# Performance work log

Measured on AMD Instinct MI355X. Metric: run time of the kernel, lower is better.

The kernel has to match this reference:

```python
import jax, jax.numpy as jnp
import numpy as np


def _rotated_kernels(kernel, n_or):
    """Nearest-neighbour rotated copies of the kernel.

    kernel: [C, kOr, kH, kW] -> returns [n_or, C, kOr, kH, kW] where slice t is the
    kernel sampled at R_{2*pi*t/n_or}(y', x') about the kernel center; rotated
    coordinates that fall outside the kernel grid contribute zero.
    """
    C, kOr, kH, kW = kernel.shape
    cy = (kH - 1) / 2.0
    cx = (kW - 1) / 2.0
    ang = 2.0 * jnp.pi * jnp.arange(n_or, dtype=jnp.float32) / n_or
    ca = jnp.cos(ang)[:, None, None]  # [n_or,1,1]
    sa = jnp.sin(ang)[:, None, None]
    yy = jnp.arange(kH, dtype=jnp.float32)[:, None] - cy  # [kH,1]
    xx = jnp.arange(kW, dtype=jnp.float32)[None, :] - cx  # [1,kW]
    # rotate grid points by angle theta
    ys = sa * xx + ca * yy  # [n_or,kH,kW]
    xs = ca * xx - sa * yy
    iy = jnp.round(ys + cy).astype(jnp.int32)
    ix = jnp.round(xs + cx).astype(jnp.int32)
    mask = ((iy >= 0) & (iy < kH) & (ix >= 0) & (ix < kW)).astype(kernel.dtype)
    iyc = jnp.clip(iy, 0, kH - 1)
    ixc = jnp.clip(ix, 0, kW - 1)
    rot = kernel[:, :, iyc, ixc]            # [C,kOr,n_or,kH,kW] (gather)
    rot = rot * mask[None, None]            # zero out-of-grid samples
    return jnp.transpose(rot, (2, 0, 1, 3, 4))  # [n_or,C,kOr,kH,kW]


def setup_inputs() -> dict:
    key = jax.random.key(0)
    k1, k2 = jax.random.split(key)
    B, C, Or, H, W = 8, 32, 8, 128, 128
    kOr, kH, kW = 8, 5, 5
    x = jax.random.normal(k1, (B, C, Or, H, W), dtype=jnp.float32)
    # module parameter: uniform(-1, 1) per reset_parameters()
    kernel = jax.random.uniform(k2, (C, kOr, kH, kW), minval=-1.0, maxval=1.0,
                                dtype=jnp.float32)
    return {"x": x, "kernel": kernel}


def reference(x, kernel):
    """SE(2) linear (depthwise) group convolution.

    out[b,c,t,y,x] = sum_{t',y',x'} x[b,c,(t+t')%Or, y+y', x+x']
                     * kernel[c, t', NN(R_{2pi t/Or}(y', x'))]
    with centered, zero-padded spatial offsets ('SAME').
    """
    B, C, Or, H, W = x.shape
    _, kOr, kH, kW = kernel.shape
    rotk = _rotated_kernels(kernel, Or)  # [Or,C,kOr,kH,kW]
    dn = ('NCHW', 'OIHW', 'NCHW')
    out = jnp.zeros((B, C * Or, H, W), dtype=x.dtype)
    for tp in range(kOr):  # small fixed orientation-offset loop
        xs = jnp.roll(x, -tp, axis=2).reshape(B, C * Or, H, W)  # circular wrap in Or
        k = jnp.transpose(rotk[:, :, tp], (1, 0, 2, 3)).reshape(C * Or, 1, kH, kW)
        out = out + jax.lax.conv_general_dilated(
            xs, k, window_strides=(1, 1), padding='SAME',
            feature_group_count=C * Or, dimension_numbers=dn)
    return out.reshape(B, C, Or, H, W)
```

## Files before the change

### kernel.cpp

```cpp
#include <hip/hip_runtime.h>


typedef short bf16x8 __attribute__((ext_vector_type(8)));
typedef float f32x4 __attribute__((ext_vector_type(4)));

#define EPIL_TS 1092
#define EPIL_RP 68

__device__ inline unsigned short f2bf(float f) {
    unsigned int u = __float_as_uint(f);
    u += 0x7fffu + ((u >> 16) & 1u);
    return (unsigned short)(u >> 16);
}
__device__ inline unsigned pk2(float a, float b) {
    return (unsigned)f2bf(a) | ((unsigned)f2bf(b) << 16);
}

__device__ __constant__ float CA8[8] = {1.0f, 0.70710678f, 0.0f, -0.70710678f,
                                        -1.0f, -0.70710678f, 0.0f, 0.70710678f};
__device__ __constant__ float SA8[8] = {0.0f, 0.70710678f, 1.0f, 0.70710678f,
                                        0.0f, -0.70710678f, -1.0f, -0.70710678f};

__device__ inline float rot_w(const float* __restrict__ kern, int c, int t,
                              int o, int dy, int dx) {
    float ca = CA8[t], sa = SA8[t];
    float xx = (float)dx - 2.0f, yy = (float)dy - 2.0f;
    int iy = (int)rintf(sa * xx + ca * yy + 2.0f);
    int ix = (int)rintf(ca * xx - sa * yy + 2.0f);
    if (iy >= 0 && iy < 5 && ix >= 0 && ix < 5) {
        int tp = (o - t) & 7;
        return kern[(c * 8 + tp) * 25 + iy * 5 + ix];
    }
    return 0.0f;
}

__global__ __launch_bounds__(256)
void build_w2(const float* __restrict__ kern, unsigned short* __restrict__ wtab) {
    int e = blockIdx.x * 256 + threadIdx.x;
    if (e >= 131072) return;
    int o   = e & 7;
    int tr  = (e >> 3) & 31;
    int n16 = (e >> 8) & 15;
    int c   = e >> 12;
    int t   = n16 & 7, dlt = n16 >> 3;
    float w = 0.0f;
    if (tr < 30) {
        int dyr = tr / 5, dx = tr - 5 * dyr;
        int dy  = dyr - dlt;
        if (dy >= 0 && dy < 5) w = rot_w(kern, c, t, o, dy, dx);
    }
    wtab[e] = f2bf(w);
}

template <bool TAB>
__global__ __launch_bounds__(256)
void se2_mfma(const float* __restrict__ x, const float* __restrict__ kern,
              const unsigned short* __restrict__ wtab, float* __restrict__ out) {
    __shared__ __align__(16) float ldsbuf[8 * EPIL_TS];
    unsigned short* stage = reinterpret_cast<unsigned short*>(ldsbuf);
    float* epil = ldsbuf;

    const int bid = (blockIdx.x & 7) * 512 + (blockIdx.x >> 3);
    const int xh2 = bid & 1;
    const int ys  = (bid >> 1) & 7;
    const int bc  = bid >> 4;
    const int c   = bc & 31;
    const int X0  = xh2 * 64, Y0 = ys * 16;
    const int tid = threadIdx.x;

    const int lane = tid & 63;
    const int wv   = tid >> 6;
    const int g    = lane >> 4;
    const int m16  = lane & 15;

    const float* xbase = x + (size_t)bc * 131072;

    auto loadch = [&](int e, float (&v)[8]) {
        int r = e / 68, col = e - r * 68;
        int gy = Y0 - 2 + r, gx = X0 - 2 + col;
        if (gy >= 0 && gy < 128 && gx >= 0 && gx < 128) {
            const float* src = xbase + gy * 128 + gx;
#pragma unroll
            for (int o = 0; o < 8; ++o) v[o] = src[o * 16384];
        } else {
#pragma unroll
            for (int o = 0; o < 8; ++o) v[o] = 0.0f;
        }
    };
    auto packch = [&](int e, const float (&v)[8]) {
        *reinterpret_cast<uint4*>(&stage[e * 8]) =
            make_uint4(pk2(v[0], v[1]), pk2(v[2], v[3]),
                       pk2(v[4], v[5]), pk2(v[6], v[7]));
    };

    float v0[8], v1[8], v2[8], v3[8], v4[8], v5[8];
    loadch(tid, v0);
    loadch(tid + 256, v1);
    loadch(tid + 512, v2);
    loadch(tid + 768, v3);
    loadch(tid + 1024, v4);
    if (tid < 80) loadch(tid + 1280, v5);

    bf16x8 wfrag[8];
    int    tapoff[8];
#pragma unroll
    for (int cc = 0; cc < 8; ++cc) {
        int tr  = cc * 4 + g;
        int trc = tr < 30 ? tr : 29;
        int dyr = trc / 5, dx = trc - 5 * dyr;
        tapoff[cc] = (dyr * 68 + dx) * 8;
        if constexpr (TAB)
            wfrag[cc] = *reinterpret_cast<const bf16x8*>(
                &wtab[((c * 16 + m16) * 32 + tr) * 8]);
    }

    if constexpr (!TAB) {
        unsigned short* ldsw = stage + 12288;
        for (int e = tid; e < 4096; e += 256) {
            int o = e & 7, tr = (e >> 3) & 31, n16 = e >> 8;
            int t = n16 & 7, dlt = n16 >> 3;
            float w = 0.0f;
            if (tr < 30) {
                int dyr = tr / 5, dx = tr - 5 * dyr;
                int dy  = dyr - dlt;
                if (dy >= 0 && dy < 5) w = rot_w(kern, c, t, o, dy, dx);
            }
            ldsw[e] = f2bf(w);
        }
        __syncthreads();
#pragma unroll
        for (int cc = 0; cc < 8; ++cc)
            wfrag[cc] = *reinterpret_cast<const bf16x8*>(
                &ldsw[(m16 * 32 + cc * 4 + g) * 8]);
        __syncthreads();
    }

    packch(tid, v0);
    packch(tid + 256, v1);
    packch(tid + 512, v2);
    packch(tid + 768, v3);
    packch(tid + 1024, v4);
    if (tid < 80) packch(tid + 1280, v5);
    __syncthreads();

    f32x4 acc[8];
#pragma unroll
    for (int s = 0; s < 8; ++s) {
        acc[s] = (f32x4){0.f, 0.f, 0.f, 0.f};
        const int yl = wv * 4 + (s >> 2) * 2;
        const int baseS = (yl * 68 + (s & 3) * 16 + m16) * 8;
#pragma unroll
        for (int cc = 0; cc < 8; ++cc) {
            bf16x8 xf = *reinterpret_cast<const bf16x8*>(&stage[baseS + tapoff[cc]]);
            acc[s] = __builtin_amdgcn_mfma_f32_16x16x32_bf16(xf, wfrag[cc], acc[s], 0, 0, 0);
        }
    }
    __syncthreads();

    const int t_o = m16 & 7, dlt = m16 >> 3;
#pragma unroll
    for (int s = 0; s < 8; ++s) {
        int y  = wv * 4 + (s >> 2) * 2 + dlt;
        int xx = (s & 3) * 16 + g * 4;
        *reinterpret_cast<f32x4*>(&epil[t_o * EPIL_TS + y * EPIL_RP + xx]) = acc[s];
    }

    float* outb = out + (size_t)bc * 131072;
#pragma unroll
    for (int j = 0; j < 8; ++j) {
        int idx = j * 64 + lane;
        int xq  = idx & 15;
        int y4  = (idx >> 4) & 3;
        int t   = idx >> 6;
        int y   = wv * 4 + y4;
        f32x4 v = *reinterpret_cast<const f32x4*>(
            &epil[t * EPIL_TS + y * EPIL_RP + xq * 4]);
        __builtin_nontemporal_store(v, reinterpret_cast<f32x4*>(
            outb + (size_t)t * 16384 + (size_t)(Y0 + y) * 128 + X0 + xq * 4));
    }
}

extern "C" void kernel_launch(void* const* d_in, const int* in_sizes, int n_in,
                              void* d_out, int out_size, void* d_ws, size_t ws_size,
                              hipStream_t stream) {
    const float* x    = (const float*)d_in[0];
    const float* kern = (const float*)d_in[1];
    float* out = (float*)d_out;
    dim3 block(256);
    if (ws_size >= 131072 * sizeof(unsigned short)) {
        unsigned short* wtab = (unsigned short*)d_ws;
        build_w2<<<dim3(512), block, 0, stream>>>(kern, wtab);
        se2_mfma<true><<<dim3(4096), block, 0, stream>>>(x, kern, wtab, out);
    } else {
        se2_mfma<false><<<dim3(4096), block, 0, stream>>>(x, kern, nullptr, out);
    }
}
```

Before: 52.35 us.

## Switch depthwise SE2 conv to 32x32x16 MFMA with 4-row output tiles

```diff
diff --git a/kernel.cpp b/kernel.cpp
--- a/kernel.cpp
+++ b/kernel.cpp
@@ -3,6 +3,7 @@
 
 typedef short bf16x8 __attribute__((ext_vector_type(8)));
 typedef float f32x4 __attribute__((ext_vector_type(4)));
+typedef float f32x16 __attribute__((ext_vector_type(16)));
 
 #define EPIL_TS 1092
 #define EPIL_RP 68
@@ -35,20 +36,17 @@
 }
 
 __global__ __launch_bounds__(256)
-void build_w2(const float* __restrict__ kern, unsigned short* __restrict__ wtab) {
+void build_w3(const float* __restrict__ kern, unsigned short* __restrict__ wtab) {
     int e = blockIdx.x * 256 + threadIdx.x;
-    if (e >= 131072) return;
-    int o   = e & 7;
-    int tr  = (e >> 3) & 31;
-    int n16 = (e >> 8) & 15;
-    int c   = e >> 12;
-    int t   = n16 & 7, dlt = n16 >> 3;
-    float w = 0.0f;
-    if (tr < 30) {
-        int dyr = tr / 5, dx = tr - 5 * dyr;
-        int dy  = dyr - dlt;
-        if (dy >= 0 && dy < 5) w = rot_w(kern, c, t, o, dy, dx);
-    }
+    if (e >= 327680) return;
+    int o  = e & 7;
+    int tr = (e >> 3) % 40;
+    int n  = (e / 320) & 31;
+    int c  = e / 10240;
+    int t  = n & 7, dlt = n >> 3;
+    int dyr = tr / 5, dx = tr - 5 * dyr;
+    int dy  = dyr - dlt;
+    float w = (dy >= 0 && dy < 5) ? rot_w(kern, c, t, o, dy, dx) : 0.0f;
     wtab[e] = f2bf(w);
 }
 
@@ -70,8 +68,9 @@
 
     const int lane = tid & 63;
     const int wv   = tid >> 6;
-    const int g    = lane >> 4;
-    const int m16  = lane & 15;
+    const int hi   = lane >> 5;
+    const int m    = lane & 31;
+    const int y_base = wv * 4;
 
     const float* xbase = x + (size_t)bc * 131072;
 
@@ -101,37 +100,22 @@
     loadch(tid + 1024, v4);
     if (tid < 80) loadch(tid + 1280, v5);
 
-    bf16x8 wfrag[8];
-    int    tapoff[8];
-#pragma unroll
-    for (int cc = 0; cc < 8; ++cc) {
-        int tr  = cc * 4 + g;
-        int trc = tr < 30 ? tr : 29;
-        int dyr = trc / 5, dx = trc - 5 * dyr;
-        tapoff[cc] = (dyr * 68 + dx) * 8;
-        if constexpr (TAB)
-            wfrag[cc] = *reinterpret_cast<const bf16x8*>(
-                &wtab[((c * 16 + m16) * 32 + tr) * 8]);
-    }
+    bf16x8 wfrag[20];
 
     if constexpr (!TAB) {
-        unsigned short* ldsw = stage + 12288;
-        for (int e = tid; e < 4096; e += 256) {
-            int o = e & 7, tr = (e >> 3) & 31, n16 = e >> 8;
-            int t = n16 & 7, dlt = n16 >> 3;
-            float w = 0.0f;
-            if (tr < 30) {
-                int dyr = tr / 5, dx = tr - 5 * dyr;
-                int dy  = dyr - dlt;
-                if (dy >= 0 && dy < 5) w = rot_w(kern, c, t, o, dy, dx);
-            }
-            ldsw[e] = f2bf(w);
+        for (int e = tid; e < 10240; e += 256) {
+            int o = e & 7, tr = (e >> 3) % 40, n2 = e / 320;
+            int t = n2 & 7, dlt = n2 >> 3;
+            int dyr = tr / 5, dx = tr - 5 * dyr;
+            int dy  = dyr - dlt;
+            float w = (dy >= 0 && dy < 5) ? rot_w(kern, c, t, o, dy, dx) : 0.0f;
+            stage[e] = f2bf(w);
         }
         __syncthreads();
 #pragma unroll
-        for (int cc = 0; cc < 8; ++cc)
-            wfrag[cc] = *reinterpret_cast<const bf16x8*>(
-                &ldsw[(m16 * 32 + cc * 4 + g) * 8]);
+        for (int s = 0; s < 20; ++s)
+            wfrag[s] = *reinterpret_cast<const bf16x8*>(
+                &stage[((m * 40) + 2 * s + hi) * 8]);
         __syncthreads();
     }
 
@@ -141,28 +125,42 @@
     packch(tid + 768, v3);
     packch(tid + 1024, v4);
     if (tid < 80) packch(tid + 1280, v5);
+
+    if constexpr (TAB) {
+        const unsigned short* wb = &wtab[((c * 32 + m) * 40 + hi) * 8];
+#pragma unroll
+        for (int s = 0; s < 20; ++s)
+            wfrag[s] = *reinterpret_cast<const bf16x8*>(&wb[s * 16]);
+    }
     __syncthreads();
 
-    f32x4 acc[8];
+    f32x16 acc0 = {0}, acc1 = {0};
+    {
+        const int baseA0 = (y_base * 68 + 0  + m) * 8;
+        const int baseA1 = (y_base * 68 + 32 + m) * 8;
 #pragma unroll
-    for (int s = 0; s < 8; ++s) {
-        acc[s] = (f32x4){0.f, 0.f, 0.f, 0.f};
-        const int yl = wv * 4 + (s >> 2) * 2;
-        const int baseS = (yl * 68 + (s & 3) * 16 + m16) * 8;
-#pragma unroll
-        for (int cc = 0; cc < 8; ++cc) {
-            bf16x8 xf = *reinterpret_cast<const bf16x8*>(&stage[baseS + tapoff[cc]]);
-            acc[s] = __builtin_amdgcn_mfma_f32_16x16x32_bf16(xf, wfrag[cc], acc[s], 0, 0, 0);
+        for (int s = 0; s < 20; ++s) {
+            const int tr0 = 2 * s, tr1 = 2 * s + 1;
+            const int t0 = ((tr0 / 5) * 68 + tr0 % 5) * 8;
+            const int t1 = ((tr1 / 5) * 68 + tr1 % 5) * 8;
+            const int toff = hi ? t1 : t0;
+            bf16x8 a0 = *reinterpret_cast<const bf16x8*>(&stage[baseA0 + toff]);
+            bf16x8 a1 = *reinterpret_cast<const bf16x8*>(&stage[baseA1 + toff]);
+            acc0 = __builtin_amdgcn_mfma_f32_32x32x16_bf16(a0, wfrag[s], acc0, 0, 0, 0);
+            acc1 = __builtin_amdgcn_mfma_f32_32x32x16_bf16(a1, wfrag[s], acc1, 0, 0, 0);
         }
     }
     __syncthreads();
 
-    const int t_o = m16 & 7, dlt = m16 >> 3;
+    const int t_o = m & 7, dlt = m >> 3;
+    const int rowb = t_o * EPIL_TS + (y_base + dlt) * EPIL_RP;
 #pragma unroll
-    for (int s = 0; s < 8; ++s) {
-        int y  = wv * 4 + (s >> 2) * 2 + dlt;
-        int xx = (s & 3) * 16 + g * 4;
-        *reinterpret_cast<f32x4*>(&epil[t_o * EPIL_TS + y * EPIL_RP + xx]) = acc[s];
+    for (int q = 0; q < 4; ++q) {
+        int xx = q * 8 + 4 * hi;
+        *reinterpret_cast<f32x4*>(&epil[rowb + xx]) =
+            (f32x4){acc0[4 * q], acc0[4 * q + 1], acc0[4 * q + 2], acc0[4 * q + 3]};
+        *reinterpret_cast<f32x4*>(&epil[rowb + 32 + xx]) =
+            (f32x4){acc1[4 * q], acc1[4 * q + 1], acc1[4 * q + 2], acc1[4 * q + 3]};
     }
 
     float* outb = out + (size_t)bc * 131072;
@@ -187,9 +185,9 @@
     const float* kern = (const float*)d_in[1];
     float* out = (float*)d_out;
     dim3 block(256);
-    if (ws_size >= 131072 * sizeof(unsigned short)) {
+    if (ws_size >= 327680 * sizeof(unsigned short)) {
         unsigned short* wtab = (unsigned short*)d_ws;
-        build_w2<<<dim3(512), block, 0, stream>>>(kern, wtab);
+        build_w3<<<dim3(1280), block, 0, stream>>>(kern, wtab);
         se2_mfma<true><<<dim3(4096), block, 0, stream>>>(x, kern, wtab, out);
     } else {
         se2_mfma<false><<<dim3(4096), block, 0, stream>>>(x, kern, nullptr, out);
```

New measurement: 65.52 us. +25.2%, slower.

## Split epilogue into per-wave staging and interleave compute with stores

Applied to the files above, without the earlier changes.

```diff
diff --git a/kernel.cpp b/kernel.cpp
--- a/kernel.cpp
+++ b/kernel.cpp
@@ -4,7 +4,7 @@
 typedef short bf16x8 __attribute__((ext_vector_type(8)));
 typedef float f32x4 __attribute__((ext_vector_type(4)));
 
-#define EPIL_TS 1092
+#define EPW 1088
 #define EPIL_RP 68
 
 __device__ inline unsigned short f2bf(float f) {
@@ -56,9 +56,8 @@
 __global__ __launch_bounds__(256)
 void se2_mfma(const float* __restrict__ x, const float* __restrict__ kern,
               const unsigned short* __restrict__ wtab, float* __restrict__ out) {
-    __shared__ __align__(16) float ldsbuf[8 * EPIL_TS];
-    unsigned short* stage = reinterpret_cast<unsigned short*>(ldsbuf);
-    float* epil = ldsbuf;
+    __shared__ __align__(16) unsigned short stage[20 * 68 * 8];
+    __shared__ __align__(16) float epil[4 * EPW];
 
     const int bid = (blockIdx.x & 7) * 512 + (blockIdx.x >> 3);
     const int xh2 = bid & 1;
@@ -115,7 +114,6 @@
     }
 
     if constexpr (!TAB) {
-        unsigned short* ldsw = stage + 12288;
         for (int e = tid; e < 4096; e += 256) {
             int o = e & 7, tr = (e >> 3) & 31, n16 = e >> 8;
             int t = n16 & 7, dlt = n16 >> 3;
@@ -125,13 +123,13 @@
                 int dy  = dyr - dlt;
                 if (dy >= 0 && dy < 5) w = rot_w(kern, c, t, o, dy, dx);
             }
-            ldsw[e] = f2bf(w);
+            stage[e] = f2bf(w);
         }
         __syncthreads();
 #pragma unroll
         for (int cc = 0; cc < 8; ++cc)
             wfrag[cc] = *reinterpret_cast<const bf16x8*>(
-                &ldsw[(m16 * 32 + cc * 4 + g) * 8]);
+                &stage[(m16 * 32 + cc * 4 + g) * 8]);
         __syncthreads();
     }
 
@@ -143,40 +141,49 @@
     if (tid < 80) packch(tid + 1280, v5);
     __syncthreads();
 
-    f32x4 acc[8];
-#pragma unroll
-    for (int s = 0; s < 8; ++s) {
-        acc[s] = (f32x4){0.f, 0.f, 0.f, 0.f};
-        const int yl = wv * 4 + (s >> 2) * 2;
-        const int baseS = (yl * 68 + (s & 3) * 16 + m16) * 8;
+    const int t_o = m16 & 7, dlt = m16 >> 3;
+    float* outb = out + (size_t)bc * 131072;
+    float* ep   = &epil[wv * EPW];
+
+#pragma unroll
+    for (int pr = 0; pr < 2; ++pr) {
+        const int yl = wv * 4 + pr * 2;
+        f32x4 acc0 = {0.f, 0.f, 0.f, 0.f};
+        f32x4 acc1 = {0.f, 0.f, 0.f, 0.f};
+        f32x4 acc2 = {0.f, 0.f, 0.f, 0.f};
+        f32x4 acc3 = {0.f, 0.f, 0.f, 0.f};
+        const int baseS = (yl * 68 + m16) * 8;
 #pragma unroll
         for (int cc = 0; cc < 8; ++cc) {
-            bf16x8 xf = *reinterpret_cast<const bf16x8*>(&stage[baseS + tapoff[cc]]);
-            acc[s] = __builtin_amdgcn_mfma_f32_16x16x32_bf16(xf, wfrag[cc], acc[s], 0, 0, 0);
-        }
-    }
-    __syncthreads();
-
-    const int t_o = m16 & 7, dlt = m16 >> 3;
-#pragma unroll
-    for (int s = 0; s < 8; ++s) {
-        int y  = wv * 4 + (s >> 2) * 2 + dlt;
-        int xx = (s & 3) * 16 + g * 4;
-        *reinterpret_cast<f32x4*>(&epil[t_o * EPIL_TS + y * EPIL_RP + xx]) = acc[s];
-    }
-
-    float* outb = out + (size_t)bc * 131072;
-#pragma unroll
-    for (int j = 0; j < 8; ++j) {
-        int idx = j * 64 + lane;
-        int xq  = idx & 15;
-        int y4  = (idx >> 4) & 3;
-        int t   = idx >> 6;
-        int y   = wv * 4 + y4;
-        f32x4 v = *reinterpret_cast<const f32x4*>(
-            &epil[t * EPIL_TS + y * EPIL_RP + xq * 4]);
-        __builtin_nontemporal_store(v, reinterpret_cast<f32x4*>(
-            outb + (size_t)t * 16384 + (size_t)(Y0 + y) * 128 + X0 + xq * 4));
+            const unsigned short* ps = &stage[baseS + tapoff[cc]];
+            bf16x8 x0 = *reinterpret_cast<const bf16x8*>(ps);
+            bf16x8 x1 = *reinterpret_cast<const bf16x8*>(ps + 128);
+            bf16x8 x2 = *reinterpret_cast<const bf16x8*>(ps + 256);
+            bf16x8 x3 = *reinterpret_cast<const bf16x8*>(ps + 384);
+            acc0 = __builtin_amdgcn_mfma_f32_16x16x32_bf16(x0, wfrag[cc], acc0, 0, 0, 0);
+            acc1 = __builtin_amdgcn_mfma_f32_16x16x32_bf16(x1, wfrag[cc], acc1, 0, 0, 0);
+            acc2 = __builtin_amdgcn_mfma_f32_16x16x32_bf16(x2, wfrag[cc], acc2, 0, 0, 0);
+            acc3 = __builtin_amdgcn_mfma_f32_16x16x32_bf16(x3, wfrag[cc], acc3, 0, 0, 0);
+        }
+
+        float* ew = ep + (t_o * 2 + dlt) * EPIL_RP;
+        *reinterpret_cast<f32x4*>(ew + 0  + g * 4) = acc0;
+        *reinterpret_cast<f32x4*>(ew + 16 + g * 4) = acc1;
+        *reinterpret_cast<f32x4*>(ew + 32 + g * 4) = acc2;
+        *reinterpret_cast<f32x4*>(ew + 48 + g * 4) = acc3;
+
+#pragma unroll
+        for (int j = 0; j < 4; ++j) {
+            int idx = j * 64 + lane;
+            int xq  = idx & 15;
+            int y2  = (idx >> 4) & 1;
+            int tt  = idx >> 5;
+            f32x4 v = *reinterpret_cast<const f32x4*>(
+                ep + (tt * 2 + y2) * EPIL_RP + xq * 4);
+            __builtin_nontemporal_store(v, reinterpret_cast<f32x4*>(
+                outb + (size_t)tt * 16384 +
+                (size_t)(Y0 + yl + y2) * 128 + X0 + xq * 4));
+        }
     }
 }
 
```

After: 51.81 us. Within noise of the previous version (-1.0%).
